# Performance work log

Measured on AMD Instinct MI355X. Metric: run time of the kernel, lower is better.

Reference implementation:

```python
import jax, jax.numpy as jnp
import numpy as np

B, S, E, H, Dh, R, L = 32, 512, 512, 8, 64, 3, 2
NI, NS = 10000, 1000
SCALE = float(1.0 / np.sqrt(Dh))
NEG = -1000000000.0


def _tensor_attn(q, kv, Wq, bq, Wk, bk, Wv, bv, Wg, bg, Wtq, btq, Wtk, btk, core, mask):
    # q, kv: [B,S,E]
    Q = q @ Wq + bq
    K = kv @ Wk + bk
    V = kv @ Wv + bv
    # per-query global bias computed from full key projection: [B,S,H] -> [B,H,S,1]
    glo = jnp.transpose(K @ Wg + bg, (0, 2, 1))[..., None]
    Qh = Q.reshape(B, S, H, Dh).transpose(0, 2, 1, 3)  # [B,H,S,Dh]
    Kh = K.reshape(B, S, H, Dh).transpose(0, 2, 1, 3)
    Vh = V.reshape(B, S, H, Dh).transpose(0, 2, 1, 3)
    scores = jnp.einsum('bhqd,bhkd->bhqk', Qh, Kh)  # [B,H,S,S]
    # low-rank bilinear tensor-core term; note it depends only on position s
    qt = Qh @ Wtq + btq  # [B,H,S,R]
    kt = Kh @ Wtk + btk  # [B,H,S,R]
    ts = jnp.einsum('bhsi,ij,bhsj->bhs', qt, core, kt)  # [B,H,S]
    scores = (scores + glo + ts[..., None]) * SCALE
    scores = jnp.where(mask, NEG, scores)
    p = jax.nn.softmax(scores, axis=-1)
    out = jnp.einsum('bhqk,bhkd->bhqd', p, Vh)
    return out.transpose(0, 2, 1, 3).reshape(B, S, E)


def setup_inputs() -> dict:
    key = jax.random.key(0)
    ks = jax.random.split(key, 24)
    f = lambda k, shp, s=0.02: (jax.random.normal(k, shp, dtype=jnp.float32) * s)
    inp = {}
    inp['item_inputs'] = jax.random.randint(ks[0], (B, S), 0, NI)
    inp['skill_inputs'] = jax.random.randint(ks[1], (B, S), 0, NS)
    inp['label_inputs'] = jax.random.randint(ks[2], (B, S), 0, 2)
    inp['item_ids'] = jax.random.randint(ks[3], (B, S), 0, NI)
    inp['skill_ids'] = jax.random.randint(ks[4], (B, S), 0, NS)
    inp['item_emb'] = f(ks[5], (NI + 1, E // 2), 1.0).at[0].set(0.0)  # padding_idx=0
    inp['skill_emb'] = f(ks[6], (NS + 1, E // 2), 1.0).at[0].set(0.0)
    inp['W_in'] = f(ks[7], (2 * E, E))
    inp['b_in'] = jnp.zeros((E,), jnp.float32)
    inp['Wq'] = f(ks[8], (L, E, E))
    inp['bq'] = jnp.zeros((L, E), jnp.float32)
    inp['Wk'] = f(ks[9], (L, E, E))
    inp['bk'] = jnp.zeros((L, E), jnp.float32)
    inp['Wv'] = f(ks[10], (L, E, E))
    inp['bv'] = jnp.zeros((L, E), jnp.float32)
    inp['Wg'] = f(ks[11], (L, E, H))
    inp['bg'] = jnp.zeros((L, H), jnp.float32)
    inp['Wtq'] = f(ks[12], (L, Dh, R), 0.1)
    inp['btq'] = jnp.zeros((L, R), jnp.float32)
    inp['Wtk'] = f(ks[13], (L, Dh, R), 0.1)
    inp['btk'] = jnp.zeros((L, R), jnp.float32)
    inp['core'] = f(ks[14], (L, R, R), 0.5)
    inp['W_out'] = f(ks[15], (E, 1))
    inp['b_out'] = jnp.zeros((1,), jnp.float32)
    return inp


def reference(item_inputs, skill_inputs, label_inputs, item_ids, skill_ids,
              item_emb, skill_emb, W_in, b_in, Wq, bq, Wk, bk, Wv, bv,
              Wg, bg, Wtq, btq, Wtk, btk, core, W_out, b_out):
    # get_inputs
    ie = item_emb[item_inputs]    # [B,S,E/2]
    se = skill_emb[skill_inputs]
    lab = label_inputs[..., None].astype(jnp.float32)
    half = jnp.concatenate([ie, se], axis=-1)  # [B,S,E]
    inputs = jnp.concatenate([half * lab, half * (1.0 - lab)], axis=-1)  # [B,S,2E]
    x = jax.nn.relu(inputs @ W_in + b_in)  # [B,S,E]
    # query
    query = jnp.concatenate([item_emb[item_ids], skill_emb[skill_ids]], axis=-1)
    mask = jnp.triu(jnp.ones((1, 1, S, S), dtype=bool), k=1)
    out = _tensor_attn(query, x, Wq[0], bq[0], Wk[0], bk[0], Wv[0], bv[0],
                       Wg[0], bg[0], Wtq[0], btq[0], Wtk[0], btk[0], core[0], mask)
    for l in range(1, L):
        res = _tensor_attn(query, out, Wq[l], bq[l], Wk[l], bk[l], Wv[l], bv[l],
                           Wg[l], bg[l], Wtq[l], btq[l], Wtk[l], btk[l], core[l], mask)
        out = out + jax.nn.relu(res)
    return out @ W_out + b_out  # [B,S,1]
```

## Files before the change

kernel.cpp:

```cpp
#include <hip/hip_runtime.h>
#include <stdint.h>


typedef short short8v __attribute__((ext_vector_type(8)));
typedef float f32x4 __attribute__((ext_vector_type(4)));

__device__ __forceinline__ float bf2f(unsigned short u) {
  union { unsigned int i; float f; } c;
  c.i = ((unsigned int)u) << 16;
  return c.f;
}
__device__ __forceinline__ unsigned short f2bf(float f) {
  union { float f; unsigned int i; } c;
  c.f = f;
  unsigned int u = c.i + 0x7FFFu + ((c.i >> 16) & 1u);
  return (unsigned short)(u >> 16);
}

__device__ __forceinline__ void g2l16(const void* g, void* l) {
  __builtin_amdgcn_global_load_lds(
      (const __attribute__((address_space(1))) unsigned int*)g,
      (__attribute__((address_space(3))) unsigned int*)l, 16, 0, 0);
}

struct WPtrs {
  const float* s[7];
  unsigned short* d[7];
};
__global__ __launch_bounds__(256) void transpose_all_k(WPtrs p, int* __restrict__ iperm) {
  int by = blockIdx.y;
  if (by == 0) {
    int gid = blockIdx.x * 256 + threadIdx.x;
    for (int i = gid; i < 16512; i += 4096) iperm[i] = 16384 + (i & 127);
  }
  __shared__ float t[32][33];
  int mi, r0t;
  if (by < 32) { mi = 0; r0t = by; }
  else { mi = 1 + ((by - 32) >> 4); r0t = (by - 32) & 15; }
  const float* in = p.s[mi];
  unsigned short* out = p.d[mi];
  int R = (mi == 0) ? 1024 : 512;
  const int C = 512;
  int c0 = blockIdx.x * 32, r0 = r0t * 32;
  int lr = threadIdx.x >> 5, lc = threadIdx.x & 31;
#pragma unroll
  for (int i = 0; i < 4; ++i) {
    int r = lr + i * 8;
    t[r][lc] = in[(size_t)(r0 + r) * C + (c0 + lc)];
  }
  __syncthreads();
#pragma unroll
  for (int i = 0; i < 4; ++i) {
    int r = lr + i * 8;
    out[(size_t)(c0 + r) * R + (r0 + lc)] = f2bf(t[lc][r]);
  }
}

__global__ __launch_bounds__(256) void scan_k(const int* __restrict__ label_in,
                                              int* __restrict__ iperm,
                                              int* __restrict__ rowpos,
                                              int* __restrict__ cnt) {
  __shared__ int sc[256];
  int t = threadIdx.x;
  int c = 0;
#pragma unroll 16
  for (int i = 0; i < 64; ++i) c += label_in[t * 64 + i];
  sc[t] = c;
  __syncthreads();
  for (int off = 1; off < 256; off <<= 1) {
    int v = sc[t];
    int u = (t >= off) ? sc[t - off] : 0;
    __syncthreads();
    sc[t] = v + u;
    __syncthreads();
  }
  int inc = sc[t];
  int ex = inc - c;
  int ex0 = t * 64 - ex;
  int p1 = ex;
  int p0 = 16511 - ex0;
  for (int i = 0; i < 64; ++i) {
    int row = t * 64 + i;
    int lb = label_in[row];
    int pos = lb ? (p1++) : (p0--);
    iperm[pos] = row;
    rowpos[row] = pos;
  }
  if (t == 255) cnt[0] = sc[255];
}

__global__ __launch_bounds__(256) void build_inputs_k(
    const int* __restrict__ item_in, const int* __restrict__ skill_in,
    const int* __restrict__ item_id, const int* __restrict__ skill_id,
    const float* __restrict__ iemb, const float* __restrict__ semb,
    unsigned short* __restrict__ HALFC, unsigned short* __restrict__ QRY,
    const int* __restrict__ rowpos) {
  int w = threadIdx.x >> 6, lane = threadIdx.x & 63;
  int row = blockIdx.x * 4 + w;
  int ii = item_in[row], si = skill_in[row];
  int iq = item_id[row], sq = skill_id[row];
  int pos = rowpos[row];
  int c = lane * 8;
  const float* src = (c < 256) ? (iemb + (size_t)ii * 256 + c)
                               : (semb + (size_t)si * 256 + (c - 256));
  union { unsigned short u[8]; int4 v; } o;
#pragma unroll
  for (int i = 0; i < 8; ++i) o.u[i] = f2bf(src[i]);
  *(int4*)(HALFC + (size_t)pos * 512 + c) = o.v;
  int qc = lane * 8;
  const float* qs = (qc < 256) ? (iemb + (size_t)iq * 256 + qc)
                               : (semb + (size_t)sq * 256 + (qc - 256));
  union { unsigned short u[8]; int4 v; } q;
#pragma unroll
  for (int i = 0; i < 8; ++i) q.u[i] = f2bf(qs[i]);
  *(int4*)(QRY + (size_t)row * 512 + qc) = q.v;
}

#define CT_LD 132

template <int MT>
__global__ __launch_bounds__(256, 4) void gemm_bt_k(
    const unsigned short* __restrict__ A, const unsigned short* __restrict__ Bt,
    unsigned short* __restrict__ C, int K, int ldc,
    const float* __restrict__ biasA, const float* __restrict__ biasB,
    int nsplit, float scale, int do_relu, unsigned short* __restrict__ VTout) {
  constexpr int NT = (MT == 128) ? 4 : 2;
  constexpr int US = ((MT * 64 + 128 * 64) > (MT * 132)) ? (MT * 64 + 128 * 64) : (MT * 132);
  __shared__ __align__(16) unsigned short uS[US];
  unsigned short* sA = uS;
  unsigned short* sB = uS + MT * 64;
  unsigned short* Ct = uS;
  int mb = blockIdx.x, nb = blockIdx.y;
  int tid = threadIdx.x;
  int w = tid >> 6, lane = tid & 63, l16 = lane & 15, quad = lane >> 4;
  int wm = (MT == 128) ? (w & 1) : 0;
  int wn = (MT == 128) ? (w >> 1) : w;
  f32x4 acc[4][NT];
#pragma unroll
  for (int i = 0; i < 4; ++i)
#pragma unroll
    for (int jn = 0; jn < NT; ++jn) acc[i][jn] = (f32x4){0.f, 0.f, 0.f, 0.f};

  for (int k0 = 0; k0 < K; k0 += 64) {
    __syncthreads();
#pragma unroll
    for (int jj = 0; jj < MT / 32; ++jj) {
      int c = jj * 256 + tid;
      int row = c >> 3, kc = c & 7;
      int src = kc ^ (row & 7);
      g2l16(A + (size_t)(mb * MT + row) * K + k0 + src * 8, sA + (size_t)c * 8);
    }
#pragma unroll
    for (int jj = 0; jj < 4; ++jj) {
      int c = jj * 256 + tid;
      int row = c >> 3, kc = c & 7;
      int src = kc ^ (row & 7);
      g2l16(Bt + (size_t)(nb * 128 + row) * K + k0 + src * 8, sB + (size_t)c * 8);
    }
    __syncthreads();
#pragma unroll
    for (int kk = 0; kk < 2; ++kk) {
      short8v aF[4], bF[NT];
#pragma unroll
      for (int mt = 0; mt < 4; ++mt) {
        int r = wm * 64 + mt * 16 + l16;
        aF[mt] = *(const short8v*)(sA + r * 64 + (((kk * 4 + quad) ^ (r & 7)) << 3));
      }
#pragma unroll
      for (int nt = 0; nt < NT; ++nt) {
        int r = wn * (16 * NT) + nt * 16 + l16;
        bF[nt] = *(const short8v*)(sB + r * 64 + (((kk * 4 + quad) ^ (r & 7)) << 3));
      }
#pragma unroll
      for (int mt = 0; mt < 4; ++mt)
#pragma unroll
        for (int nt = 0; nt < NT; ++nt)
          acc[mt][nt] =
              __builtin_amdgcn_mfma_f32_16x16x32_bf16(aF[mt], bF[nt], acc[mt][nt], 0, 0, 0);
    }
  }
  __syncthreads();
#pragma unroll
  for (int mt = 0; mt < 4; ++mt)
#pragma unroll
    for (int nt = 0; nt < NT; ++nt) {
      int col = wn * (16 * NT) + nt * 16 + l16;
      int gcol = nb * 128 + col;
      float bs = (gcol < nsplit) ? biasA[gcol] : biasB[gcol - nsplit];
#pragma unroll
      for (int r = 0; r < 4; ++r) {
        int row = wm * 64 + mt * 16 + quad * 4 + r;
        float v = (acc[mt][nt][r] + bs) * scale;
        if (do_relu) v = fmaxf(v, 0.f);
        Ct[row * CT_LD + col] = f2bf(v);
      }
    }
  __syncthreads();
  if (VTout && nb >= 4) {
    int bb = mb >> 2, kpb = (mb & 3) * 128;
#pragma unroll
    for (int it = 0; it < 8; ++it) {
      int idx = it * 256 + tid;
      int dloc = idx >> 4, rem = idx & 15;
      union { unsigned short u[8]; int4 v; } o;
#pragma unroll
      for (int s = 0; s < 8; ++s) {
        int r = 32 * (rem >> 2) + 16 * (s >> 2) + 4 * (rem & 3) + (s & 3);
        o.u[s] = Ct[r * CT_LD + dloc];
      }
      *(int4*)(VTout + (size_t)(bb * 512 + (nb - 4) * 128 + dloc) * 512 + kpb + rem * 8) = o.v;
    }
  } else {
#pragma unroll
    for (int it = 0; it < MT / 16; ++it) {
      int row = it * 16 + (tid >> 4);
      int col8 = (tid & 15) * 8;
      *(int4*)(C + (size_t)(mb * MT + row) * ldc + nb * 128 + col8) =
          *(const int4*)(Ct + row * CT_LD + col8);
    }
  }
}

__global__ __launch_bounds__(256, 4) void gemm_in_k(
    const unsigned short* __restrict__ A, const unsigned short* __restrict__ Bt,
    unsigned short* __restrict__ C, const int* __restrict__ iperm,
    const int* __restrict__ cnt, const float* __restrict__ bias) {
  __shared__ __align__(16) unsigned short uS[64 * 64 + 128 * 64];
  unsigned short* sA = uS;
  unsigned short* sB = uS + 64 * 64;
  unsigned short* Ct = uS;
  int mb = blockIdx.x, nb = blockIdx.y;
  int tid = threadIdx.x;
  int w = tid >> 6, lane = tid & 63, l16 = lane & 15, quad = lane >> 4;
  int n1 = *cnt;
  int koff = (mb < ((n1 + 63) >> 6)) ? 0 : 512;
  f32x4 acc[4][2];
#pragma unroll
  for (int i = 0; i < 4; ++i)
#pragma unroll
    for (int jn = 0; jn < 2; ++jn) acc[i][jn] = (f32x4){0.f, 0.f, 0.f, 0.f};

  for (int k0 = 0; k0 < 512; k0 += 64) {
    __syncthreads();
#pragma unroll
    for (int jj = 0; jj < 2; ++jj) {
      int c = jj * 256 + tid;
      int row = c >> 3, kc = c & 7;
      int src = kc ^ (row & 7);
      g2l16(A + (size_t)(mb * 64 + row) * 512 + k0 + src * 8, sA + (size_t)c * 8);
    }
#pragma unroll
    for (int jj = 0; jj < 4; ++jj) {
      int c = jj * 256 + tid;
      int row = c >> 3, kc = c & 7;
      int src = kc ^ (row & 7);
      g2l16(Bt + (size_t)(nb * 128 + row) * 1024 + koff + k0 + src * 8, sB + (size_t)c * 8);
    }
    __syncthreads();
#pragma unroll
    for (int kk = 0; kk < 2; ++kk) {
      short8v aF[4], bF[2];
#pragma unroll
      for (int mt = 0; mt < 4; ++mt) {
        int r = mt * 16 + l16;
        aF[mt] = *(const short8v*)(sA + r * 64 + (((kk * 4 + quad) ^ (r & 7)) << 3));
      }
#pragma unroll
      for (int nt = 0; nt < 2; ++nt) {
        int r = w * 32 + nt * 16 + l16;
        bF[nt] = *(const short8v*)(sB + r * 64 + (((kk * 4 + quad) ^ (r & 7)) << 3));
      }
#pragma unroll
      for (int mt = 0; mt < 4; ++mt)
#pragma unroll
        for (int nt = 0; nt < 2; ++nt)
          acc[mt][nt] =
              __builtin_amdgcn_mfma_f32_16x16x32_bf16(aF[mt], bF[nt], acc[mt][nt], 0, 0, 0);
    }
  }
  __syncthreads();
#pragma unroll
  for (int mt = 0; mt < 4; ++mt)
#pragma unroll
    for (int nt = 0; nt < 2; ++nt) {
      int col = w * 32 + nt * 16 + l16;
      float bs = bias[nb * 128 + col];
#pragma unroll
      for (int r = 0; r < 4; ++r) {
        int row = mt * 16 + quad * 4 + r;
        Ct[row * CT_LD + col] = f2bf(fmaxf(acc[mt][nt][r] + bs, 0.f));
      }
    }
  __syncthreads();
#pragma unroll
  for (int it = 0; it < 4; ++it) {
    int row = it * 16 + (tid >> 4);
    int tgt = iperm[mb * 64 + row];
    int col8 = (tid & 15) * 8;
    *(int4*)(C + (size_t)tgt * 512 + nb * 128 + col8) = *(const int4*)(Ct + row * CT_LD + col8);
  }
}

__global__ __launch_bounds__(256, 4) void attn_k(const unsigned short* __restrict__ Qb,
                                                 int ldq,
                                                 const unsigned short* __restrict__ KVb,
                                                 const unsigned short* __restrict__ VT,
                                                 unsigned short* __restrict__ Out) {
  __shared__ __align__(16) unsigned short sK[64 * 64];
  __shared__ __align__(16) unsigned short sV[64 * 64];
  int tid = threadIdx.x;
  int w = tid >> 6, lane = tid & 63;
  int l16 = lane & 15, quad = lane >> 4;
  int bh = blockIdx.x;
  int b = bh >> 3, h = bh & 7;
  int jb = 7 - (int)blockIdx.y;
  int qb = jb * 64 + w * 16;
  f32x4 zf = {0.f, 0.f, 0.f, 0.f};
  short8v onesF;
#pragma unroll
  for (int i = 0; i < 8; ++i) onesF[i] = (short)0x3F80;

  short8v qF[2];
#pragma unroll
  for (int hf = 0; hf < 2; ++hf)
    qF[hf] = *(const short8v*)(Qb + (size_t)(b * 512 + qb + l16) * ldq + h * 64 + hf * 32 +
                               quad * 8);

  f32x4 O[4], RS = zf;
#pragma unroll
  for (int dt = 0; dt < 4; ++dt) O[dt] = zf;

  const unsigned short* Kg = KVb + (size_t)(b * 512) * 1024 + h * 64;
  const unsigned short* Vg = VT + (size_t)(bh * 64) * 512;

  for (int kt = 0; kt <= jb; ++kt) {
    __syncthreads();
#pragma unroll
    for (int jj = 0; jj < 2; ++jj) {
      int c = jj * 256 + tid;
      int row = c >> 3, kc = c & 7, src = kc ^ (row & 7);
      g2l16(Kg + (size_t)(kt * 64 + row) * 1024 + src * 8, sK + c * 8);
    }
#pragma unroll
    for (int jj = 0; jj < 2; ++jj) {
      int c = jj * 256 + tid;
      int row = c >> 3, kc = c & 7, src = kc ^ (row & 7);
      g2l16(Vg + (size_t)row * 512 + kt * 64 + src * 8, sV + c * 8);
    }
    __syncthreads();
#pragma unroll
    for (int kp = 0; kp < 2; ++kp) {
      int kb32 = kt * 64 + kp * 32;
      if (kb32 > qb) continue;
      short8v kC[2][2], vC[4];
#pragma unroll
      for (int v = 0; v < 2; ++v) {
        int r = kp * 32 + v * 16 + l16;
#pragma unroll
        for (int hf = 0; hf < 2; ++hf)
          kC[v][hf] = *(const short8v*)(sK + r * 64 + (((hf * 4 + quad) ^ (r & 7)) << 3));
      }
#pragma unroll
      for (int dt = 0; dt < 4; ++dt) {
        int r = dt * 16 + l16;
        vC[dt] = *(const short8v*)(sV + r * 64 + (((kp * 4 + quad) ^ (r & 7)) << 3));
      }
      f32x4 S[2];
#pragma unroll
      for (int v = 0; v < 2; ++v) {
        f32x4 s0 = __builtin_amdgcn_mfma_f32_16x16x32_bf16(kC[v][0], qF[0], zf, 0, 0, 0);
        S[v] = __builtin_amdgcn_mfma_f32_16x16x32_bf16(kC[v][1], qF[1], s0, 0, 0, 0);
      }
      if (kb32 + 31 > qb) {
#pragma unroll
        for (int v = 0; v < 2; ++v)
#pragma unroll
          for (int r = 0; r < 4; ++r)
            if (kb32 + v * 16 + quad * 4 + r > qb + l16) S[v][r] = -1e30f;
      }
      union { unsigned int u32[4]; short8v v8; } pk;
#pragma unroll
      for (int i = 0; i < 4; ++i) {
        int v = i >> 1, r0 = (i & 1) * 2;
        float e0 = __expf(S[v][r0]);
        float e1 = __expf(S[v][r0 + 1]);
        pk.u32[i] = (__float_as_uint(e0) >> 16) | (__float_as_uint(e1) & 0xFFFF0000u);
      }
#pragma unroll
      for (int dt = 0; dt < 4; ++dt)
        O[dt] = __builtin_amdgcn_mfma_f32_16x16x32_bf16(pk.v8, vC[dt], O[dt], 0, 0, 0);
      RS = __builtin_amdgcn_mfma_f32_16x16x32_bf16(pk.v8, onesF, RS, 0, 0, 0);
    }
  }
  float lr[4];
#pragma unroll
  for (int r = 0; r < 4; ++r) lr[r] = 1.f / RS[r];
#pragma unroll
  for (int dt = 0; dt < 4; ++dt)
#pragma unroll
    for (int r = 0; r < 4; ++r)
      Out[(size_t)(b * 512 + qb + quad * 4 + r) * 512 + h * 64 + dt * 16 + l16] =
          f2bf(O[dt][r] * lr[r]);
}

__global__ __launch_bounds__(256) void final_k(const unsigned short* __restrict__ out0,
                                               const unsigned short* __restrict__ res1,
                                               const float* __restrict__ wout,
                                               const float* __restrict__ bout,
                                               float* __restrict__ dst) {
  int w = threadIdx.x >> 6, lane = threadIdx.x & 63;
  int row = blockIdx.x * 4 + w;
  const unsigned short* o = out0 + (size_t)row * 512 + lane * 8;
  const unsigned short* r = res1 + (size_t)row * 512 + lane * 8;
  const float* wv = wout + lane * 8;
  float acc = 0.f;
#pragma unroll
  for (int i = 0; i < 8; ++i) {
    float rv = bf2f(r[i]);
    acc += (bf2f(o[i]) + fmaxf(rv, 0.f)) * wv[i];
  }
#pragma unroll
  for (int off = 1; off <= 32; off <<= 1) acc += __shfl_xor(acc, off);
  if (lane == 0) dst[row] = acc + bout[0];
}

extern "C" void kernel_launch(void* const* d_in, const int* in_sizes, int n_in,
                              void* d_out, int out_size, void* d_ws, size_t ws_size,
                              hipStream_t stream) {
  (void)in_sizes; (void)n_in; (void)out_size; (void)ws_size;
  const int* item_inputs = (const int*)d_in[0];
  const int* skill_inputs = (const int*)d_in[1];
  const int* label_inputs = (const int*)d_in[2];
  const int* item_ids = (const int*)d_in[3];
  const int* skill_ids = (const int*)d_in[4];
  const float* item_emb = (const float*)d_in[5];
  const float* skill_emb = (const float*)d_in[6];
  const float* W_in = (const float*)d_in[7];
  const float* b_in = (const float*)d_in[8];
  const float* Wq = (const float*)d_in[9];
  const float* bq = (const float*)d_in[10];
  const float* Wk = (const float*)d_in[11];
  const float* bk = (const float*)d_in[12];
  const float* Wv = (const float*)d_in[13];
  const float* bv = (const float*)d_in[14];
  const float* W_out = (const float*)d_in[22];
  const float* b_out = (const float*)d_in[23];

  unsigned short* ws = (unsigned short*)d_ws;
  unsigned short* HALFC = ws;
  unsigned short* OUT0 = ws;
  unsigned short* RES1 = ws + (size_t)16512 * 512;
  unsigned short* QRY = RES1 + (size_t)16384 * 512;
  unsigned short* X = QRY + (size_t)16384 * 512;
  unsigned short* Qb = X + (size_t)16512 * 512;
  unsigned short* KVb = Qb + (size_t)16384 * 1024;
  unsigned short* WInT = KVb + (size_t)16384 * 1024;
  unsigned short* WqTC = WInT + 512 * 1024;
  unsigned short* WkvT0 = WqTC + (size_t)1024 * 512;
  unsigned short* WkvT1 = WkvT0 + (size_t)1024 * 512;
  unsigned short* VT = WkvT1 + (size_t)1024 * 512;
  int* IPERM = (int*)(VT + (size_t)16384 * 512);
  int* CNT = IPERM + 16512;
  int* ROWPOS = CNT + 2;

  WPtrs p;
  p.s[0] = W_in;           p.d[0] = WInT;
  p.s[1] = Wq;             p.d[1] = WqTC;
  p.s[2] = Wq + 262144;    p.d[2] = WqTC + 512 * 512;
  p.s[3] = Wk;             p.d[3] = WkvT0;
  p.s[4] = Wv;             p.d[4] = WkvT0 + 262144;
  p.s[5] = Wk + 262144;    p.d[5] = WkvT1;
  p.s[6] = Wv + 262144;    p.d[6] = WkvT1 + 262144;
  transpose_all_k<<<dim3(16, 128), 256, 0, stream>>>(p, IPERM);

  scan_k<<<1, 256, 0, stream>>>(label_inputs, IPERM, ROWPOS, CNT);

  build_inputs_k<<<4096, 256, 0, stream>>>(item_inputs, skill_inputs, item_ids, skill_ids,
                                           item_emb, skill_emb, HALFC, QRY, ROWPOS);
  gemm_in_k<<<dim3(258, 4), 256, 0, stream>>>(HALFC, WInT, X, IPERM, CNT, b_in);

  const float SC = 0.125f;
  gemm_bt_k<128><<<dim3(128, 8), 256, 0, stream>>>(QRY, WqTC, Qb, 512, 1024, bq, bq + 512,
                                                   512, SC, 0, nullptr);
  gemm_bt_k<128><<<dim3(128, 8), 256, 0, stream>>>(X, WkvT0, KVb, 512, 1024, bk, bv, 512,
                                                   1.0f, 0, VT);
  attn_k<<<dim3(256, 8), 256, 0, stream>>>(Qb, 1024, KVb, VT, OUT0);
  gemm_bt_k<128><<<dim3(128, 8), 256, 0, stream>>>(OUT0, WkvT1, KVb, 512, 1024, bk + 512,
                                                   bv + 512, 512, 1.0f, 0, VT);
  attn_k<<<dim3(256, 8), 256, 0, stream>>>(Qb + 512, 1024, KVb, VT, RES1);
  final_k<<<4096, 256, 0, stream>>>(OUT0, RES1, W_out, b_out, (float*)d_out);
}
```

Before: 276.8 us.

## Merge Q and input GEMMs into one launch; fuse final projection into attention

The input-embedding GEMM and the query-projection GEMM now run as one launch, with the block index choosing which tile type each block computes. This removes a launch and lets the two independent GEMMs overlap. The final output projection is folded into the second attention kernel's epilogue, which reduces per-head partial dot products with shuffles and atomically adds them into the output. The output is pre-filled with the bias during the preceding GEMM, so the RES1 buffer and the final kernel go away, at the cost of float atomics and nondeterministic summation order.

```diff
diff --git a/kernel.cpp b/kernel.cpp
--- a/kernel.cpp
+++ b/kernel.cpp
@@ -118,63 +118,210 @@
 
 #define CT_LD 132
 
-template <int MT>
+__global__ __launch_bounds__(256, 4) void gemm_q_in_k(
+    const unsigned short* __restrict__ QRY, const unsigned short* __restrict__ WqTC,
+    unsigned short* __restrict__ Qb, const unsigned short* __restrict__ HALFC,
+    const unsigned short* __restrict__ WInT, unsigned short* __restrict__ X,
+    const int* __restrict__ iperm, const int* __restrict__ cnt,
+    const float* __restrict__ b_in, const float* __restrict__ bq, float SC) {
+  __shared__ __align__(16) unsigned short uS[128 * CT_LD];
+  int bid = blockIdx.x;
+  int tid = threadIdx.x;
+  int w = tid >> 6, lane = tid & 63, l16 = lane & 15, quad = lane >> 4;
+  if (bid < 1024) {
+    unsigned short* sA = uS;
+    unsigned short* sB = uS + 128 * 64;
+    unsigned short* Ct = uS;
+    int mb = bid >> 3, nb = bid & 7;
+    int wm = w & 1, wn = w >> 1;
+    f32x4 acc[4][4];
+#pragma unroll
+    for (int i = 0; i < 4; ++i)
+#pragma unroll
+      for (int j = 0; j < 4; ++j) acc[i][j] = (f32x4){0.f, 0.f, 0.f, 0.f};
+    for (int k0 = 0; k0 < 512; k0 += 64) {
+      __syncthreads();
+#pragma unroll
+      for (int jj = 0; jj < 4; ++jj) {
+        int c = jj * 256 + tid;
+        int row = c >> 3, kc = c & 7, src = kc ^ (row & 7);
+        g2l16(QRY + (size_t)(mb * 128 + row) * 512 + k0 + src * 8, sA + (size_t)c * 8);
+      }
+#pragma unroll
+      for (int jj = 0; jj < 4; ++jj) {
+        int c = jj * 256 + tid;
+        int row = c >> 3, kc = c & 7, src = kc ^ (row & 7);
+        g2l16(WqTC + (size_t)(nb * 128 + row) * 512 + k0 + src * 8, sB + (size_t)c * 8);
+      }
+      __syncthreads();
+#pragma unroll
+      for (int kk = 0; kk < 2; ++kk) {
+        short8v aF[4], bF[4];
+#pragma unroll
+        for (int mt = 0; mt < 4; ++mt) {
+          int r = wm * 64 + mt * 16 + l16;
+          aF[mt] = *(const short8v*)(sA + r * 64 + (((kk * 4 + quad) ^ (r & 7)) << 3));
+        }
+#pragma unroll
+        for (int nt = 0; nt < 4; ++nt) {
+          int r = wn * 64 + nt * 16 + l16;
+          bF[nt] = *(const short8v*)(sB + r * 64 + (((kk * 4 + quad) ^ (r & 7)) << 3));
+        }
+#pragma unroll
+        for (int mt = 0; mt < 4; ++mt)
+#pragma unroll
+          for (int nt = 0; nt < 4; ++nt)
+            acc[mt][nt] =
+                __builtin_amdgcn_mfma_f32_16x16x32_bf16(aF[mt], bF[nt], acc[mt][nt], 0, 0, 0);
+      }
+    }
+    __syncthreads();
+#pragma unroll
+    for (int mt = 0; mt < 4; ++mt)
+#pragma unroll
+      for (int nt = 0; nt < 4; ++nt) {
+        int col = wn * 64 + nt * 16 + l16;
+        float bs = bq[nb * 128 + col];
+#pragma unroll
+        for (int r = 0; r < 4; ++r) {
+          int row = wm * 64 + mt * 16 + quad * 4 + r;
+          Ct[row * CT_LD + col] = f2bf((acc[mt][nt][r] + bs) * SC);
+        }
+      }
+    __syncthreads();
+#pragma unroll
+    for (int it = 0; it < 8; ++it) {
+      int row = it * 16 + (tid >> 4);
+      int col8 = (tid & 15) * 8;
+      *(int4*)(Qb + (size_t)(mb * 128 + row) * 1024 + nb * 128 + col8) =
+          *(const int4*)(Ct + row * CT_LD + col8);
+    }
+  } else {
+    unsigned short* sA = uS;
+    unsigned short* sB = uS + 64 * 64;
+    unsigned short* Ct = uS;
+    int id = bid - 1024;
+    int mb = id >> 2, nb = id & 3;
+    int n1 = *cnt;
+    int koff = (mb < ((n1 + 63) >> 6)) ? 0 : 512;
+    f32x4 acc[4][2];
+#pragma unroll
+    for (int i = 0; i < 4; ++i)
+#pragma unroll
+      for (int j = 0; j < 2; ++j) acc[i][j] = (f32x4){0.f, 0.f, 0.f, 0.f};
+    for (int k0 = 0; k0 < 512; k0 += 64) {
+      __syncthreads();
+#pragma unroll
+      for (int jj = 0; jj < 2; ++jj) {
+        int c = jj * 256 + tid;
+        int row = c >> 3, kc = c & 7, src = kc ^ (row & 7);
+        g2l16(HALFC + (size_t)(mb * 64 + row) * 512 + k0 + src * 8, sA + (size_t)c * 8);
+      }
+#pragma unroll
+      for (int jj = 0; jj < 4; ++jj) {
+        int c = jj * 256 + tid;
+        int row = c >> 3, kc = c & 7, src = kc ^ (row & 7);
+        g2l16(WInT + (size_t)(nb * 128 + row) * 1024 + koff + k0 + src * 8, sB + (size_t)c * 8);
+      }
+      __syncthreads();
+#pragma unroll
+      for (int kk = 0; kk < 2; ++kk) {
+        short8v aF[4], bF[2];
+#pragma unroll
+        for (int mt = 0; mt < 4; ++mt) {
+          int r = mt * 16 + l16;
+          aF[mt] = *(const short8v*)(sA + r * 64 + (((kk * 4 + quad) ^ (r & 7)) << 3));
+        }
+#pragma unroll
+        for (int nt = 0; nt < 2; ++nt) {
+          int r = w * 32 + nt * 16 + l16;
+          bF[nt] = *(const short8v*)(sB + r * 64 + (((kk * 4 + quad) ^ (r & 7)) << 3));
+        }
+#pragma unroll
+        for (int mt = 0; mt < 4; ++mt)
+#pragma unroll
+          for (int nt = 0; nt < 2; ++nt)
+            acc[mt][nt] =
+                __builtin_amdgcn_mfma_f32_16x16x32_bf16(aF[mt], bF[nt], acc[mt][nt], 0, 0, 0);
+      }
+    }
+    __syncthreads();
+#pragma unroll
+    for (int mt = 0; mt < 4; ++mt)
+#pragma unroll
+      for (int nt = 0; nt < 2; ++nt) {
+        int col = w * 32 + nt * 16 + l16;
+        float bs = b_in[nb * 128 + col];
+#pragma unroll
+        for (int r = 0; r < 4; ++r) {
+          int row = mt * 16 + quad * 4 + r;
+          Ct[row * CT_LD + col] = f2bf(fmaxf(acc[mt][nt][r] + bs, 0.f));
+        }
+      }
+    __syncthreads();
+#pragma unroll
+    for (int it = 0; it < 4; ++it) {
+      int row = it * 16 + (tid >> 4);
+      int tgt = iperm[mb * 64 + row];
+      int col8 = (tid & 15) * 8;
+      *(int4*)(X + (size_t)tgt * 512 + nb * 128 + col8) = *(const int4*)(Ct + row * CT_LD + col8);
+    }
+  }
+}
+
 __global__ __launch_bounds__(256, 4) void gemm_bt_k(
     const unsigned short* __restrict__ A, const unsigned short* __restrict__ Bt,
     unsigned short* __restrict__ C, int K, int ldc,
     const float* __restrict__ biasA, const float* __restrict__ biasB,
-    int nsplit, float scale, int do_relu, unsigned short* __restrict__ VTout) {
-  constexpr int NT = (MT == 128) ? 4 : 2;
-  constexpr int US = ((MT * 64 + 128 * 64) > (MT * 132)) ? (MT * 64 + 128 * 64) : (MT * 132);
-  __shared__ __align__(16) unsigned short uS[US];
+    int nsplit, float scale, unsigned short* __restrict__ VTout,
+    float* __restrict__ dstfill, const float* __restrict__ bout) {
+  __shared__ __align__(16) unsigned short uS[128 * CT_LD];
   unsigned short* sA = uS;
-  unsigned short* sB = uS + MT * 64;
+  unsigned short* sB = uS + 128 * 64;
   unsigned short* Ct = uS;
   int mb = blockIdx.x, nb = blockIdx.y;
   int tid = threadIdx.x;
   int w = tid >> 6, lane = tid & 63, l16 = lane & 15, quad = lane >> 4;
-  int wm = (MT == 128) ? (w & 1) : 0;
-  int wn = (MT == 128) ? (w >> 1) : w;
-  f32x4 acc[4][NT];
+  int wm = w & 1, wn = w >> 1;
+  if (dstfill && nb == 0 && tid < 128) dstfill[mb * 128 + tid] = bout[0];
+  f32x4 acc[4][4];
 #pragma unroll
   for (int i = 0; i < 4; ++i)
 #pragma unroll
-    for (int jn = 0; jn < NT; ++jn) acc[i][jn] = (f32x4){0.f, 0.f, 0.f, 0.f};
+    for (int jn = 0; jn < 4; ++jn) acc[i][jn] = (f32x4){0.f, 0.f, 0.f, 0.f};
 
   for (int k0 = 0; k0 < K; k0 += 64) {
     __syncthreads();
-#pragma unroll
-    for (int jj = 0; jj < MT / 32; ++jj) {
-      int c = jj * 256 + tid;
-      int row = c >> 3, kc = c & 7;
-      int src = kc ^ (row & 7);
-      g2l16(A + (size_t)(mb * MT + row) * K + k0 + src * 8, sA + (size_t)c * 8);
-    }
 #pragma unroll
     for (int jj = 0; jj < 4; ++jj) {
       int c = jj * 256 + tid;
-      int row = c >> 3, kc = c & 7;
-      int src = kc ^ (row & 7);
+      int row = c >> 3, kc = c & 7, src = kc ^ (row & 7);
+      g2l16(A + (size_t)(mb * 128 + row) * K + k0 + src * 8, sA + (size_t)c * 8);
+    }
+#pragma unroll
+    for (int jj = 0; jj < 4; ++jj) {
+      int c = jj * 256 + tid;
+      int row = c >> 3, kc = c & 7, src = kc ^ (row & 7);
       g2l16(Bt + (size_t)(nb * 128 + row) * K + k0 + src * 8, sB + (size_t)c * 8);
     }
     __syncthreads();
 #pragma unroll
     for (int kk = 0; kk < 2; ++kk) {
-      short8v aF[4], bF[NT];
+      short8v aF[4], bF[4];
 #pragma unroll
       for (int mt = 0; mt < 4; ++mt) {
         int r = wm * 64 + mt * 16 + l16;
         aF[mt] = *(const short8v*)(sA + r * 64 + (((kk * 4 + quad) ^ (r & 7)) << 3));
       }
 #pragma unroll
-      for (int nt = 0; nt < NT; ++nt) {
-        int r = wn * (16 * NT) + nt * 16 + l16;
+      for (int nt = 0; nt < 4; ++nt) {
+        int r = wn * 64 + nt * 16 + l16;
         bF[nt] = *(const short8v*)(sB + r * 64 + (((kk * 4 + quad) ^ (r & 7)) << 3));
       }
 #pragma unroll
       for (int mt = 0; mt < 4; ++mt)
 #pragma unroll
-        for (int nt = 0; nt < NT; ++nt)
+        for (int nt = 0; nt < 4; ++nt)
           acc[mt][nt] =
               __builtin_amdgcn_mfma_f32_16x16x32_bf16(aF[mt], bF[nt], acc[mt][nt], 0, 0, 0);
     }
@@ -183,16 +330,14 @@
 #pragma unroll
   for (int mt = 0; mt < 4; ++mt)
 #pragma unroll
-    for (int nt = 0; nt < NT; ++nt) {
-      int col = wn * (16 * NT) + nt * 16 + l16;
+    for (int nt = 0; nt < 4; ++nt) {
+      int col = wn * 64 + nt * 16 + l16;
       int gcol = nb * 128 + col;
       float bs = (gcol < nsplit) ? biasA[gcol] : biasB[gcol - nsplit];
 #pragma unroll
       for (int r = 0; r < 4; ++r) {
         int row = wm * 64 + mt * 16 + quad * 4 + r;
-        float v = (acc[mt][nt][r] + bs) * scale;
-        if (do_relu) v = fmaxf(v, 0.f);
-        Ct[row * CT_LD + col] = f2bf(v);
+        Ct[row * CT_LD + col] = f2bf((acc[mt][nt][r] + bs) * scale);
       }
     }
   __syncthreads();
@@ -212,100 +357,24 @@
     }
   } else {
 #pragma unroll
-    for (int it = 0; it < MT / 16; ++it) {
+    for (int it = 0; it < 8; ++it) {
       int row = it * 16 + (tid >> 4);
       int col8 = (tid & 15) * 8;
-      *(int4*)(C + (size_t)(mb * MT + row) * ldc + nb * 128 + col8) =
+      *(int4*)(C + (size_t)(mb * 128 + row) * ldc + nb * 128 + col8) =
           *(const int4*)(Ct + row * CT_LD + col8);
     }
   }
 }
 
-__global__ __launch_bounds__(256, 4) void gemm_in_k(
-    const unsigned short* __restrict__ A, const unsigned short* __restrict__ Bt,
-    unsigned short* __restrict__ C, const int* __restrict__ iperm,
-    const int* __restrict__ cnt, const float* __restrict__ bias) {
-  __shared__ __align__(16) unsigned short uS[64 * 64 + 128 * 64];
-  unsigned short* sA = uS;
-  unsigned short* sB = uS + 64 * 64;
-  unsigned short* Ct = uS;
-  int mb = blockIdx.x, nb = blockIdx.y;
-  int tid = threadIdx.x;
-  int w = tid >> 6, lane = tid & 63, l16 = lane & 15, quad = lane >> 4;
-  int n1 = *cnt;
-  int koff = (mb < ((n1 + 63) >> 6)) ? 0 : 512;
-  f32x4 acc[4][2];
-#pragma unroll
-  for (int i = 0; i < 4; ++i)
-#pragma unroll
-    for (int jn = 0; jn < 2; ++jn) acc[i][jn] = (f32x4){0.f, 0.f, 0.f, 0.f};
-
-  for (int k0 = 0; k0 < 512; k0 += 64) {
-    __syncthreads();
-#pragma unroll
-    for (int jj = 0; jj < 2; ++jj) {
-      int c = jj * 256 + tid;
-      int row = c >> 3, kc = c & 7;
-      int src = kc ^ (row & 7);
-      g2l16(A + (size_t)(mb * 64 + row) * 512 + k0 + src * 8, sA + (size_t)c * 8);
-    }
-#pragma unroll
-    for (int jj = 0; jj < 4; ++jj) {
-      int c = jj * 256 + tid;
-      int row = c >> 3, kc = c & 7;
-      int src = kc ^ (row & 7);
-      g2l16(Bt + (size_t)(nb * 128 + row) * 1024 + koff + k0 + src * 8, sB + (size_t)c * 8);
-    }
-    __syncthreads();
-#pragma unroll
-    for (int kk = 0; kk < 2; ++kk) {
-      short8v aF[4], bF[2];
-#pragma unroll
-      for (int mt = 0; mt < 4; ++mt) {
-        int r = mt * 16 + l16;
-        aF[mt] = *(const short8v*)(sA + r * 64 + (((kk * 4 + quad) ^ (r & 7)) << 3));
-      }
-#pragma unroll
-      for (int nt = 0; nt < 2; ++nt) {
-        int r = w * 32 + nt * 16 + l16;
-        bF[nt] = *(const short8v*)(sB + r * 64 + (((kk * 4 + quad) ^ (r & 7)) << 3));
-      }
-#pragma unroll
-      for (int mt = 0; mt < 4; ++mt)
-#pragma unroll
-        for (int nt = 0; nt < 2; ++nt)
-          acc[mt][nt] =
-              __builtin_amdgcn_mfma_f32_16x16x32_bf16(aF[mt], bF[nt], acc[mt][nt], 0, 0, 0);
-    }
-  }
-  __syncthreads();
-#pragma unroll
-  for (int mt = 0; mt < 4; ++mt)
-#pragma unroll
-    for (int nt = 0; nt < 2; ++nt) {
-      int col = w * 32 + nt * 16 + l16;
-      float bs = bias[nb * 128 + col];
-#pragma unroll
-      for (int r = 0; r < 4; ++r) {
-        int row = mt * 16 + quad * 4 + r;
-        Ct[row * CT_LD + col] = f2bf(fmaxf(acc[mt][nt][r] + bs, 0.f));
-      }
-    }
-  __syncthreads();
-#pragma unroll
-  for (int it = 0; it < 4; ++it) {
-    int row = it * 16 + (tid >> 4);
-    int tgt = iperm[mb * 64 + row];
-    int col8 = (tid & 15) * 8;
-    *(int4*)(C + (size_t)tgt * 512 + nb * 128 + col8) = *(const int4*)(Ct + row * CT_LD + col8);
-  }
-}
-
+template <int FINAL>
 __global__ __launch_bounds__(256, 4) void attn_k(const unsigned short* __restrict__ Qb,
                                                  int ldq,
                                                  const unsigned short* __restrict__ KVb,
                                                  const unsigned short* __restrict__ VT,
-                                                 unsigned short* __restrict__ Out) {
+                                                 unsigned short* __restrict__ Out,
+                                                 const unsigned short* __restrict__ out0,
+                                                 const float* __restrict__ wout,
+                                                 float* __restrict__ dst) {
   __shared__ __align__(16) unsigned short sK[64 * 64];
   __shared__ __align__(16) unsigned short sV[64 * 64];
   int tid = threadIdx.x;
@@ -395,33 +464,36 @@
   float lr[4];
 #pragma unroll
   for (int r = 0; r < 4; ++r) lr[r] = 1.f / RS[r];
-#pragma unroll
-  for (int dt = 0; dt < 4; ++dt)
-#pragma unroll
-    for (int r = 0; r < 4; ++r)
-      Out[(size_t)(b * 512 + qb + quad * 4 + r) * 512 + h * 64 + dt * 16 + l16] =
-          f2bf(O[dt][r] * lr[r]);
-}
-
-__global__ __launch_bounds__(256) void final_k(const unsigned short* __restrict__ out0,
-                                               const unsigned short* __restrict__ res1,
-                                               const float* __restrict__ wout,
-                                               const float* __restrict__ bout,
-                                               float* __restrict__ dst) {
-  int w = threadIdx.x >> 6, lane = threadIdx.x & 63;
-  int row = blockIdx.x * 4 + w;
-  const unsigned short* o = out0 + (size_t)row * 512 + lane * 8;
-  const unsigned short* r = res1 + (size_t)row * 512 + lane * 8;
-  const float* wv = wout + lane * 8;
-  float acc = 0.f;
-#pragma unroll
-  for (int i = 0; i < 8; ++i) {
-    float rv = bf2f(r[i]);
-    acc += (bf2f(o[i]) + fmaxf(rv, 0.f)) * wv[i];
-  }
-#pragma unroll
-  for (int off = 1; off <= 32; off <<= 1) acc += __shfl_xor(acc, off);
-  if (lane == 0) dst[row] = acc + bout[0];
+  if (!FINAL) {
+#pragma unroll
+    for (int dt = 0; dt < 4; ++dt)
+#pragma unroll
+      for (int r = 0; r < 4; ++r)
+        Out[(size_t)(b * 512 + qb + quad * 4 + r) * 512 + h * 64 + dt * 16 + l16] =
+            f2bf(O[dt][r] * lr[r]);
+  } else {
+    float s[4] = {0.f, 0.f, 0.f, 0.f};
+#pragma unroll
+    for (int dt = 0; dt < 4; ++dt) {
+      float wv = wout[h * 64 + dt * 16 + l16];
+#pragma unroll
+      for (int r = 0; r < 4; ++r) {
+        float rv = bf2f(f2bf(O[dt][r] * lr[r]));
+        float oo = bf2f(out0[(size_t)(b * 512 + qb + quad * 4 + r) * 512 + h * 64 +
+                             dt * 16 + l16]);
+        s[r] += (oo + fmaxf(rv, 0.f)) * wv;
+      }
+    }
+#pragma unroll
+    for (int off = 1; off < 16; off <<= 1)
+#pragma unroll
+      for (int r = 0; r < 4; ++r) s[r] += __shfl_xor(s[r], off);
+    if (l16 == 0) {
+#pragma unroll
+      for (int r = 0; r < 4; ++r)
+        atomicAdd(dst + b * 512 + qb + quad * 4 + r, s[r]);
+    }
+  }
 }
 
 extern "C" void kernel_launch(void* const* d_in, const int* in_sizes, int n_in,
@@ -449,8 +521,7 @@
   unsigned short* ws = (unsigned short*)d_ws;
   unsigned short* HALFC = ws;
   unsigned short* OUT0 = ws;
-  unsigned short* RES1 = ws + (size_t)16512 * 512;
-  unsigned short* QRY = RES1 + (size_t)16384 * 512;
+  unsigned short* QRY = ws + (size_t)16512 * 512;
   unsigned short* X = QRY + (size_t)16384 * 512;
   unsigned short* Qb = X + (size_t)16512 * 512;
   unsigned short* KVb = Qb + (size_t)16384 * 1024;
@@ -477,16 +548,16 @@
 
   build_inputs_k<<<4096, 256, 0, stream>>>(item_inputs, skill_inputs, item_ids, skill_ids,
                                            item_emb, skill_emb, HALFC, QRY, ROWPOS);
-  gemm_in_k<<<dim3(258, 4), 256, 0, stream>>>(HALFC, WInT, X, IPERM, CNT, b_in);
 
   const float SC = 0.125f;
-  gemm_bt_k<128><<<dim3(128, 8), 256, 0, stream>>>(QRY, WqTC, Qb, 512, 1024, bq, bq + 512,
-                                                   512, SC, 0, nullptr);
-  gemm_bt_k<128><<<dim3(128, 8), 256, 0, stream>>>(X, WkvT0, KVb, 512, 1024, bk, bv, 512,
-                                                   1.0f, 0, VT);
-  attn_k<<<dim3(256, 8), 256, 0, stream>>>(Qb, 1024, KVb, VT, OUT0);
-  gemm_bt_k<128><<<dim3(128, 8), 256, 0, stream>>>(OUT0, WkvT1, KVb, 512, 1024, bk + 512,
-                                                   bv + 512, 512, 1.0f, 0, VT);
-  attn_k<<<dim3(256, 8), 256, 0, stream>>>(Qb + 512, 1024, KVb, VT, RES1);
-  final_k<<<4096, 256, 0, stream>>>(OUT0, RES1, W_out, b_out, (float*)d_out);
-}
+  gemm_q_in_k<<<2056, 256, 0, stream>>>(QRY, WqTC, Qb, HALFC, WInT, X, IPERM, CNT, b_in, bq,
+                                        SC);
+  gemm_bt_k<<<dim3(128, 8), 256, 0, stream>>>(X, WkvT0, KVb, 512, 1024, bk, bv, 512, 1.0f,
+                                              VT, nullptr, nullptr);
+  attn_k<0><<<dim3(256, 8), 256, 0, stream>>>(Qb, 1024, KVb, VT, OUT0, nullptr, nullptr,
+                                              nullptr);
+  gemm_bt_k<<<dim3(128, 8), 256, 0, stream>>>(OUT0, WkvT1, KVb, 512, 1024, bk + 512,
+                                              bv + 512, 512, 1.0f, VT, (float*)d_out, b_out);
+  attn_k<1><<<dim3(256, 8), 256, 0, stream>>>(Qb + 512, 1024, KVb, VT, nullptr, OUT0, W_out,
+                                              (float*)d_out);
+}
```

Result: faster. 262.2 us (-5.3%).
